# Optimization experiments

Hardware: AMD Instinct MI355X
Metric: run time of the kernel (lower is better)

Reference implementation:

```python
import jax, jax.numpy as jnp
import numpy as np

D = 256      # d_model
H = 8        # num heads
HD = D // H  # head dim
DFF = 1024   # feedforward dim
S = 1024     # seq len
B = 8        # batch
EPS = 1e-5


def _layernorm(x, g, b):
    mu = jnp.mean(x, axis=-1, keepdims=True)
    var = jnp.mean((x - mu) ** 2, axis=-1, keepdims=True)
    return (x - mu) * jax.lax.rsqrt(var + EPS) * g + b


def setup_inputs() -> dict:
    key = jax.random.key(0)
    ks = jax.random.split(key, 12)
    xav = lambda k, shape: jax.random.uniform(
        k, shape, jnp.float32, -1.0, 1.0) * np.sqrt(6.0 / (shape[0] + shape[-1]))
    return {
        "src": jax.random.normal(ks[0], (S, B, D), jnp.float32),
        "bias": jax.random.normal(ks[1], (B, H, S, S), jnp.float32),
        "in_proj_w": xav(ks[2], (3 * D, D)),
        "in_proj_b": jnp.zeros((3 * D,), jnp.float32),
        "out_w": xav(ks[3], (D, D)),
        "out_b": jnp.zeros((D,), jnp.float32),
        "w1": xav(ks[4], (DFF, D)),
        "b1": jnp.zeros((DFF,), jnp.float32),
        "w2": xav(ks[5], (D, DFF)),
        "b2": jnp.zeros((D,), jnp.float32),
        "g1": jnp.ones((D,), jnp.float32),
        "be1": jnp.zeros((D,), jnp.float32),
        "g2": jnp.ones((D,), jnp.float32),
        "be2": jnp.zeros((D,), jnp.float32),
    }


def reference(src, bias, in_proj_w, in_proj_b, out_w, out_b,
              w1, b1, w2, b2, g1, be1, g2, be2):
    # Pre-norm (note: residual uses the NORMED src, matching the torch code)
    x = _layernorm(src, g1, be1)                       # [S,B,D]
    qkv = x @ in_proj_w.T + in_proj_b                  # [S,B,3D]
    q, k, v = jnp.split(qkv, 3, axis=-1)
    q = q * (HD ** -0.5)
    # [S,B,D] -> [B,H,S,HD]
    to_heads = lambda t: t.reshape(S, B, H, HD).transpose(1, 2, 0, 3)
    qh, kh, vh = to_heads(q), to_heads(k), to_heads(v)
    scores = jnp.einsum('bhsd,bhtd->bhst', qh, kh) + bias
    attn = jax.nn.softmax(scores, axis=-1)             # [B,H,S,S]
    ctx = jnp.einsum('bhst,bhtd->bhsd', attn, vh)      # [B,H,S,HD]
    ctx = ctx.transpose(2, 0, 1, 3).reshape(S, B, D)
    attn_out = ctx @ out_w.T + out_b
    x = x + attn_out                                   # residual (eval: no dropout)
    y = _layernorm(x, g2, be2)
    ff = jax.nn.relu(y @ w1.T + b1) @ w2.T + b2
    return y + ff
```

## Files before the change

kernel.cpp:

```cpp
#include <hip/hip_runtime.h>
#include <hip/hip_bf16.h>
#include <cstdint>

typedef unsigned short u16;
typedef __attribute__((ext_vector_type(8))) short bf16x8;
typedef __attribute__((ext_vector_type(4))) float f32x4;

#define S_LEN 1024
#define BATCH 8
#define DMODEL 256
#define NHEAD 8
#define HDIM 32
#define DFF 1024
#define NROWS (S_LEN * BATCH)

static __device__ __forceinline__ u16 f2b(float f) {
    union { float f; unsigned u; } x{f};
    unsigned r = (x.u + 0x7fffu + ((x.u >> 16) & 1u)) >> 16;
    return (u16)r;
}

__global__ __launch_bounds__(256) void prep_kernel(
    const float* __restrict__ in, const float* __restrict__ g1,
    const float* __restrict__ be1, float* __restrict__ of, u16* __restrict__ ob,
    const float* __restrict__ ipw, const float* __restrict__ outw,
    const float* __restrict__ w1, const float* __restrict__ w2,
    const float* __restrict__ ipb,
    u16* __restrict__ wqkv, u16* __restrict__ wout,
    u16* __restrict__ w1b, u16* __restrict__ w2b, float* __restrict__ bq)
{
    const float s = 0.17677669529663689f;
    if (blockIdx.x >= 2048) {
        const int i4 = ((int)blockIdx.x - 2048) * 1024 + threadIdx.x * 4;
        const float* src; u16* dst; int off; float sc = 1.0f;
        if (i4 < 196608)      { src = ipw;  dst = wqkv; off = 0;      if (i4 < 65536) sc = s; }
        else if (i4 < 262144) { src = outw; dst = wout; off = 196608; }
        else if (i4 < 524288) { src = w1;   dst = w1b;  off = 262144; }
        else                  { src = w2;   dst = w2b;  off = 524288; }
        const float4 v = *(const float4*)(src + i4 - off);
        uint2 pk;
        pk.x = (unsigned)f2b(v.x * sc) | ((unsigned)f2b(v.y * sc) << 16);
        pk.y = (unsigned)f2b(v.z * sc) | ((unsigned)f2b(v.w * sc) << 16);
        *(uint2*)(dst + i4 - off) = pk;
        if (i4 < 768) {
            const float4 b = *(const float4*)(ipb + i4);
            const float bs = (i4 < 256) ? s : 1.0f;
            *(float4*)(bq + i4) = make_float4(b.x * bs, b.y * bs, b.z * bs, b.w * bs);
        }
        return;
    }
    const int w = threadIdx.x >> 6, l = threadIdx.x & 63;
    const int row = blockIdx.x * 4 + w;
    const float4 v = *(const float4*)(in + (size_t)row * DMODEL + l * 4);
    float s0 = v.x + v.y + v.z + v.w;
    #pragma unroll
    for (int o = 32; o; o >>= 1) s0 += __shfl_xor(s0, o);
    const float mu = s0 * (1.0f / DMODEL);
    const float dx = v.x - mu, dy = v.y - mu, dz = v.z - mu, dw = v.w - mu;
    float sq = dx * dx + dy * dy + dz * dz + dw * dw;
    #pragma unroll
    for (int o = 32; o; o >>= 1) sq += __shfl_xor(sq, o);
    const float rs = rsqrtf(sq * (1.0f / DMODEL) + 1e-5f);
    const float4 gv = *(const float4*)(g1 + l * 4);
    const float4 bv = *(const float4*)(be1 + l * 4);
    const float r0 = dx * rs * gv.x + bv.x;
    const float r1 = dy * rs * gv.y + bv.y;
    const float r2 = dz * rs * gv.z + bv.z;
    const float r3 = dw * rs * gv.w + bv.w;
    *(float4*)(of + (size_t)row * DMODEL + l * 4) = make_float4(r0, r1, r2, r3);
    uint2 pk;
    pk.x = (unsigned)f2b(r0) | ((unsigned)f2b(r1) << 16);
    pk.y = (unsigned)f2b(r2) | ((unsigned)f2b(r3) << 16);
    *(uint2*)(ob + (size_t)row * DMODEL + l * 4) = pk;
}

template <int MF>
__device__ __forceinline__ void gemm_core(
    const u16* __restrict__ A, const u16* __restrict__ Bw,
    int N, int K, int nbase, int rowbase, u16* sB, f32x4 acc[MF][4])
{
    const int tid = threadIdx.x, w = tid >> 6, l = tid & 63;
    const int g = l >> 4, q = l & 15;
    const u16* Arow = A + (size_t)(rowbase + w * (MF * 16) + q) * K + g * 8;

    const int sbr = tid >> 3, sseg = tid & 7;
    const size_t bsrc0 = (size_t)(nbase + sbr) * K + sseg * 8;
    const size_t bsrc1 = (size_t)(nbase + sbr + 32) * K + sseg * 8;
    const int d0 = sbr * 128 + ((sseg * 16) ^ ((sbr & 7) << 4));
    const int d1 = d0 + 32 * 128;

    {
        const uint4 r0 = *(const uint4*)(Bw + bsrc0);
        const uint4 r1 = *(const uint4*)(Bw + bsrc1);
        *(uint4*)((char*)sB + d0) = r0;
        *(uint4*)((char*)sB + d1) = r1;
    }
    const int NC = K >> 6;
    for (int c = 0; c < NC; ++c) {
        __syncthreads();
        char* sBc = (char*)sB + (c & 1) * 8192;
        char* sBn = (char*)sB + ((c + 1) & 1) * 8192;
        uint4 p0, p1;
        if (c + 1 < NC) {
            p0 = *(const uint4*)(Bw + bsrc0 + (c + 1) * 64);
            p1 = *(const uint4*)(Bw + bsrc1 + (c + 1) * 64);
        }
        const int kk = c * 64;
        #pragma unroll
        for (int ks = 0; ks < 2; ++ks) {
            bf16x8 af[MF];
            #pragma unroll
            for (int m = 0; m < MF; ++m)
                af[m] = *(const bf16x8*)(Arow + (size_t)m * 16 * K + kk + ks * 32);
            #pragma unroll
            for (int n = 0; n < 4; ++n) {
                const int rr = n * 16 + q;
                const bf16x8 bf = *(const bf16x8*)(
                    sBc + rr * 128 + ((ks * 64 + g * 16) ^ ((rr & 7) << 4)));
                #pragma unroll
                for (int m = 0; m < MF; ++m)
                    acc[m][n] = __builtin_amdgcn_mfma_f32_16x16x32_bf16(bf, af[m], acc[m][n], 0, 0, 0);
            }
        }
        if (c + 1 < NC) {
            *(uint4*)(sBn + d0) = p0;
            *(uint4*)(sBn + d1) = p1;
        }
    }
}

__global__ __launch_bounds__(256) void gemm_qkv(
    const u16* __restrict__ A, const u16* __restrict__ Bw,
    const float* __restrict__ bias,
    u16* __restrict__ Qh, u16* __restrict__ Kh, u16* __restrict__ Vt)
{
    __shared__ u16 sB[2][64 * 64];
    const int tid = threadIdx.x, w = tid >> 6, l = tid & 63;
    const int g = l >> 4, q = l & 15;
    const int rowbase = blockIdx.x * 128, nbase = blockIdx.y * 64;
    f32x4 acc[2][4] = {};
    gemm_core<2>(A, Bw, 768, 256, nbase, rowbase, &sB[0][0], acc);

    #pragma unroll
    for (int m = 0; m < 2; ++m) {
        const int row = rowbase + w * 32 + m * 16 + q;
        const int s = row >> 3, b = row & 7;
        if (nbase < 512) {
            u16* dst = (nbase >= 256) ? Kh : Qh;
            #pragma unroll
            for (int n = 0; n < 4; ++n) {
                const int col = nbase + n * 16 + g * 4;
                const float4 bv = *(const float4*)(bias + col);
                const int cc = col & 255, h = cc >> 5, hd = cc & 31;
                const int bh = b * 8 + h;
                uint2 pk;
                pk.x = (unsigned)f2b(acc[m][n][0] + bv.x) | ((unsigned)f2b(acc[m][n][1] + bv.y) << 16);
                pk.y = (unsigned)f2b(acc[m][n][2] + bv.z) | ((unsigned)f2b(acc[m][n][3] + bv.w) << 16);
                *(uint2*)(dst + ((size_t)bh * S_LEN + s) * HDIM + hd) = pk;
            }
        } else {
            #pragma unroll
            for (int n = 0; n < 4; ++n) {
                const int col = nbase + n * 16 + g * 4;
                const float4 bv = *(const float4*)(bias + col);
                const int cc = col - 512, h = cc >> 5, hd = cc & 31;
                const int bh = b * 8 + h;
                Vt[((size_t)bh * HDIM + hd + 0) * S_LEN + s] = f2b(acc[m][n][0] + bv.x);
                Vt[((size_t)bh * HDIM + hd + 1) * S_LEN + s] = f2b(acc[m][n][1] + bv.y);
                Vt[((size_t)bh * HDIM + hd + 2) * S_LEN + s] = f2b(acc[m][n][2] + bv.z);
                Vt[((size_t)bh * HDIM + hd + 3) * S_LEN + s] = f2b(acc[m][n][3] + bv.w);
            }
        }
    }
}

template <int MODE, int MF>
__global__ __launch_bounds__(256) void gemm_nt(
    const u16* __restrict__ A, const u16* __restrict__ Bw,
    const float* __restrict__ bias, const float* __restrict__ resid,
    float* __restrict__ outf, u16* __restrict__ outb,
    int N, int K)
{
    __shared__ u16 sB[2][64 * 64];
    const int tid = threadIdx.x, w = tid >> 6, l = tid & 63;
    const int g = l >> 4, q = l & 15;
    const int rowbase = blockIdx.x * (MF * 64), nbase = blockIdx.y * 64;
    f32x4 acc[MF][4] = {};
    gemm_core<MF>(A, Bw, N, K, nbase, rowbase, &sB[0][0], acc);

    #pragma unroll
    for (int m = 0; m < MF; ++m) {
        const int row = rowbase + w * (MF * 16) + m * 16 + q;
        #pragma unroll
        for (int n = 0; n < 4; ++n) {
            const int col = nbase + n * 16 + g * 4;
            const float4 bv = *(const float4*)(bias + col);
            float v0 = acc[m][n][0] + bv.x, v1 = acc[m][n][1] + bv.y;
            float v2 = acc[m][n][2] + bv.z, v3 = acc[m][n][3] + bv.w;
            if (MODE == 2) {
                v0 = fmaxf(v0, 0.f); v1 = fmaxf(v1, 0.f);
                v2 = fmaxf(v2, 0.f); v3 = fmaxf(v3, 0.f);
                uint2 pk;
                pk.x = (unsigned)f2b(v0) | ((unsigned)f2b(v1) << 16);
                pk.y = (unsigned)f2b(v2) | ((unsigned)f2b(v3) << 16);
                *(uint2*)(outb + (size_t)row * N + col) = pk;
            } else {
                const float4 rv = *(const float4*)(resid + (size_t)row * N + col);
                *(float4*)(outf + (size_t)row * N + col) =
                    make_float4(v0 + rv.x, v1 + rv.y, v2 + rv.z, v3 + rv.w);
            }
        }
    }
}

__global__ __launch_bounds__(256) void attn_kernel(
    const u16* __restrict__ Qh, const u16* __restrict__ Kh,
    const u16* __restrict__ Vt, const float* __restrict__ bias,
    u16* __restrict__ ctx)
{
    __shared__ u16 sK[2][64 * 32];
    __shared__ u16 sV[2][32 * 64];
    __shared__ u16 sP[4][16 * 64];
    const int tid = threadIdx.x, w = tid >> 6, l = tid & 63;
    const int g = l >> 4, q = l & 15;
    const int bh = blockIdx.y, b = bh >> 3, h = bh & 7;
    const int qbase = blockIdx.x * 64 + w * 16;
    const int qrow = qbase + q;

    const bf16x8 qf = *(const bf16x8*)(Qh + ((size_t)bh * S_LEN + qrow) * HDIM + g * 8);
    const float* brow = bias + ((size_t)bh * S_LEN + qrow) * S_LEN;
    u16* Pw = sP[w];
    const int swz = (q & 7) << 4;

    const u16* KsrcBase = Kh + ((size_t)bh * S_LEN + w * 16 + q) * HDIM + g * 8;
    const u16* VsrcBase = Vt + ((size_t)bh * HDIM + (w & 1) * 16 + q) * S_LEN
                             + (w >> 1) * 32 + g * 8;
    u16* KdstA = &sK[0][tid * 8]; u16* KdstB = &sK[1][tid * 8];
    u16* VdstA = &sV[0][tid * 8]; u16* VdstB = &sV[1][tid * 8];

    f32x4 ctxa[2] = {{0,0,0,0},{0,0,0,0}};
    float m = -1e30f, lsum = 0.f;

    auto loadB = [&](int kt, f32x4* bv) {
        #pragma unroll
        for (int n = 0; n < 4; ++n)
            bv[n] = __builtin_nontemporal_load(
                (const f32x4*)(brow + kt * 64 + n * 16 + g * 4));
    };

    auto proc = [&](int buf, const f32x4* bv) {
        f32x4 sc[4];
        #pragma unroll
        for (int n = 0; n < 4; ++n) {
            const bf16x8 kf = *(const bf16x8*)(&sK[buf][(n * 64 + l) * 8]);
            f32x4 z = {0, 0, 0, 0};
            sc[n] = __builtin_amdgcn_mfma_f32_16x16x32_bf16(kf, qf, z, 0, 0, 0);
        }
        #pragma unroll
        for (int n = 0; n < 4; ++n)
            #pragma unroll
            for (int r = 0; r < 4; ++r) sc[n][r] += bv[n][r];

        float mx = sc[0][0];
        #pragma unroll
        for (int n = 0; n < 4; ++n)
            #pragma unroll
            for (int r = 0; r < 4; ++r) mx = fmaxf(mx, sc[n][r]);
        mx = fmaxf(mx, __shfl_xor(mx, 16));
        mx = fmaxf(mx, __shfl_xor(mx, 32));
        const float mn = fmaxf(m, mx);
        const float corr = __expf(m - mn);
        float su = 0.f;
        u16 pb[16];
        #pragma unroll
        for (int n = 0; n < 4; ++n)
            #pragma unroll
            for (int r = 0; r < 4; ++r) {
                const float pv = __expf(sc[n][r] - mn);
                su += pv;
                pb[n * 4 + r] = f2b(pv);
            }
        su += __shfl_xor(su, 16);
        su += __shfl_xor(su, 32);
        lsum = lsum * corr + su;
        m = mn;
        #pragma unroll
        for (int jg = 0; jg < 2; ++jg)
            #pragma unroll
            for (int r = 0; r < 4; ++r) ctxa[jg][r] *= corr;

        #pragma unroll
        for (int n = 0; n < 4; ++n) {
            uint2 pk;
            pk.x = (unsigned)pb[n * 4] | ((unsigned)pb[n * 4 + 1] << 16);
            pk.y = (unsigned)pb[n * 4 + 2] | ((unsigned)pb[n * 4 + 3] << 16);
            *(uint2*)((char*)Pw + q * 128 + ((n * 32 + g * 8) ^ swz)) = pk;
        }

        #pragma unroll
        for (int ks = 0; ks < 2; ++ks) {
            const bf16x8 pf = *(const bf16x8*)((char*)Pw + q * 128 + ((ks * 64 + g * 16) ^ swz));
            #pragma unroll
            for (int jg = 0; jg < 2; ++jg) {
                const bf16x8 vf = *(const bf16x8*)(&sV[buf][((ks * 2 + jg) * 64 + l) * 8]);
                ctxa[jg] = __builtin_amdgcn_mfma_f32_16x16x32_bf16(vf, pf, ctxa[jg], 0, 0, 0);
            }
        }
    };

    f32x4 bv0[4], bv1[4];
    {
        const uint4 kr = *(const uint4*)(KsrcBase);
        const uint4 vr = *(const uint4*)(VsrcBase);
        *(uint4*)KdstA = kr;
        *(uint4*)VdstA = vr;
        loadB(0, bv0);
    }
    __syncthreads();

    for (int kt = 0; kt < 16; kt += 2) {
        {
            uint4 kr, vr;
            kr = *(const uint4*)(KsrcBase + (size_t)(kt + 1) * 64 * HDIM);
            vr = *(const uint4*)(VsrcBase + (size_t)(kt + 1) * 64);
            loadB(kt + 1, bv1);
            proc(0, bv0);
            *(uint4*)KdstB = kr;
            *(uint4*)VdstB = vr;
        }
        __syncthreads();
        {
            uint4 kr, vr;
            if (kt + 2 < 16) {
                kr = *(const uint4*)(KsrcBase + (size_t)(kt + 2) * 64 * HDIM);
                vr = *(const uint4*)(VsrcBase + (size_t)(kt + 2) * 64);
                loadB(kt + 2, bv0);
            }
            proc(1, bv1);
            if (kt + 2 < 16) {
                *(uint4*)KdstA = kr;
                *(uint4*)VdstA = vr;
            }
        }
        __syncthreads();
    }

    const float inv = 1.0f / lsum;
    #pragma unroll
    for (int jg = 0; jg < 2; ++jg) {
        uint2 pk;
        pk.x = (unsigned)f2b(ctxa[jg][0] * inv) | ((unsigned)f2b(ctxa[jg][1] * inv) << 16);
        pk.y = (unsigned)f2b(ctxa[jg][2] * inv) | ((unsigned)f2b(ctxa[jg][3] * inv) << 16);
        *(uint2*)(ctx + ((size_t)qrow * 8 + b) * DMODEL + h * 32 + jg * 16 + g * 4) = pk;
    }
}

__global__ __launch_bounds__(256) void oproj_ln(
    const u16* __restrict__ ctx, const u16* __restrict__ wob,
    const float* __restrict__ ob, const float* __restrict__ xf,
    const float* __restrict__ g2, const float* __restrict__ be2,
    float* __restrict__ yf, u16* __restrict__ yb)
{
    __shared__ float s1[4][16], s2[4][16];
    const int tid = threadIdx.x, wv = tid >> 6, l = tid & 63;
    const int g = l >> 4, q = l & 15;
    const int row = blockIdx.x * 16 + q;
    f32x4 acc[4] = {{0,0,0,0},{0,0,0,0},{0,0,0,0},{0,0,0,0}};
    const u16* Arow = ctx + (size_t)row * 256 + g * 8;
    const u16* Brow = wob + (size_t)(wv * 64 + q) * 256 + g * 8;

    #pragma unroll 2
    for (int kk = 0; kk < 256; kk += 32) {
        const bf16x8 af = *(const bf16x8*)(Arow + kk);
        #pragma unroll
        for (int n = 0; n < 4; ++n) {
            const bf16x8 bf = *(const bf16x8*)(Brow + (size_t)n * 16 * 256 + kk);
            acc[n] = __builtin_amdgcn_mfma_f32_16x16x32_bf16(bf, af, acc[n], 0, 0, 0);
        }
    }

    float sum = 0.f;
    #pragma unroll
    for (int n = 0; n < 4; ++n) {
        const int col = wv * 64 + n * 16 + g * 4;
        const float4 bv = *(const float4*)(ob + col);
        const float4 rv = *(const float4*)(xf + (size_t)row * 256 + col);
        acc[n][0] += bv.x + rv.x; acc[n][1] += bv.y + rv.y;
        acc[n][2] += bv.z + rv.z; acc[n][3] += bv.w + rv.w;
        sum += acc[n][0] + acc[n][1] + acc[n][2] + acc[n][3];
    }
    sum += __shfl_xor(sum, 16);
    sum += __shfl_xor(sum, 32);
    if (l < 16) s1[wv][q] = sum;
    __syncthreads();
    const float mu = (s1[0][q] + s1[1][q] + s1[2][q] + s1[3][q]) * (1.0f / 256);
    float sq = 0.f;
    #pragma unroll
    for (int n = 0; n < 4; ++n)
        #pragma unroll
        for (int r = 0; r < 4; ++r) {
            const float d = acc[n][r] - mu;
            sq += d * d;
        }
    sq += __shfl_xor(sq, 16);
    sq += __shfl_xor(sq, 32);
    if (l < 16) s2[wv][q] = sq;
    __syncthreads();
    const float rs = rsqrtf((s2[0][q] + s2[1][q] + s2[2][q] + s2[3][q]) * (1.0f / 256) + 1e-5f);

    #pragma unroll
    for (int n = 0; n < 4; ++n) {
        const int col = wv * 64 + n * 16 + g * 4;
        const float4 gv = *(const float4*)(g2 + col);
        const float4 b2 = *(const float4*)(be2 + col);
        const float y0 = (acc[n][0] - mu) * rs * gv.x + b2.x;
        const float y1 = (acc[n][1] - mu) * rs * gv.y + b2.y;
        const float y2 = (acc[n][2] - mu) * rs * gv.z + b2.z;
        const float y3 = (acc[n][3] - mu) * rs * gv.w + b2.w;
        *(float4*)(yf + (size_t)row * 256 + col) = make_float4(y0, y1, y2, y3);
        uint2 pk;
        pk.x = (unsigned)f2b(y0) | ((unsigned)f2b(y1) << 16);
        pk.y = (unsigned)f2b(y2) | ((unsigned)f2b(y3) << 16);
        *(uint2*)(yb + (size_t)row * 256 + col) = pk;
    }
}

extern "C" void kernel_launch(void* const* d_in, const int* in_sizes, int n_in,
                              void* d_out, int out_size, void* d_ws, size_t ws_size,
                              hipStream_t stream)
{
    const float* src  = (const float*)d_in[0];
    const float* bias = (const float*)d_in[1];
    const float* ipw  = (const float*)d_in[2];
    const float* ipb  = (const float*)d_in[3];
    const float* outw = (const float*)d_in[4];
    const float* outb = (const float*)d_in[5];
    const float* w1   = (const float*)d_in[6];
    const float* b1   = (const float*)d_in[7];
    const float* w2   = (const float*)d_in[8];
    const float* b2   = (const float*)d_in[9];
    const float* g1   = (const float*)d_in[10];
    const float* be1  = (const float*)d_in[11];
    const float* g2   = (const float*)d_in[12];
    const float* be2  = (const float*)d_in[13];

    char* p = (char*)d_ws;
    auto alloc = [&](size_t bytes) -> void* {
        void* r = (void*)p;
        p += (bytes + 255) & ~(size_t)255;
        return r;
    };
    float* xf   = (float*)alloc((size_t)NROWS * DMODEL * 4);
    u16*   xb   = (u16*)  alloc((size_t)NROWS * DMODEL * 2);
    u16*   Qh   = (u16*)  alloc((size_t)64 * S_LEN * HDIM * 2);
    u16*   Kb   = (u16*)  alloc((size_t)64 * S_LEN * HDIM * 2);
    u16*   Vt   = (u16*)  alloc((size_t)64 * S_LEN * HDIM * 2);
    u16*   ctx  = (u16*)  alloc((size_t)NROWS * DMODEL * 2);
    float* yf   = (float*)alloc((size_t)NROWS * DMODEL * 4);
    u16*   yb   = (u16*)  alloc((size_t)NROWS * DMODEL * 2);
    u16*   hb   = (u16*)  alloc((size_t)NROWS * DFF * 2);
    u16*   wqkv = (u16*)  alloc((size_t)768 * 256 * 2);
    u16*   wob  = (u16*)  alloc((size_t)256 * 256 * 2);
    u16*   w1b  = (u16*)  alloc((size_t)1024 * 256 * 2);
    u16*   w2b  = (u16*)  alloc((size_t)256 * 1024 * 2);
    float* bq   = (float*)alloc(768 * 4);

    prep_kernel<<<2816, 256, 0, stream>>>(src, g1, be1, xf, xb,
                                          ipw, outw, w1, w2, ipb,
                                          wqkv, wob, w1b, w2b, bq);
    gemm_qkv<<<dim3(64, 12), 256, 0, stream>>>(xb, wqkv, bq, Qh, Kb, Vt);
    attn_kernel<<<dim3(16, 64), 256, 0, stream>>>(Qh, Kb, Vt, bias, ctx);
    oproj_ln<<<512, 256, 0, stream>>>(ctx, wob, outb, xf, g2, be2, yf, yb);
    gemm_nt<2, 2><<<dim3(64, 16), 256, 0, stream>>>(yb, w1b, b1, nullptr, nullptr, hb, 1024, 256);
    gemm_nt<3, 1><<<dim3(128, 4), 256, 0, stream>>>(hb, w2b, b2, yf, (float*)d_out, nullptr, 256, 1024);
}
```

Before: 157.3 us.

## Fuse FFN up and down projections through shared memory; widen oproj tiles

Replaces the two separate FFN GEMM launches with one kernel. Each 512-thread block computes a 32-row slice of the ReLU hidden activations into a swizzled 64KB LDS buffer, then immediately runs the down-projection with the residual add. This removes the global round-trip of the 8192x1024 bf16 hidden tensor and one launch. The output-projection+LayerNorm kernel now handles 32 rows per block instead of 16. The trade-offs are only 256 blocks, large LDS per block limiting occupancy, and B operands read directly from global without LDS staging.

```diff
diff --git a/kernel.cpp b/kernel.cpp
--- a/kernel.cpp
+++ b/kernel.cpp
@@ -174,45 +174,6 @@
     }
 }
 
-template <int MODE, int MF>
-__global__ __launch_bounds__(256) void gemm_nt(
-    const u16* __restrict__ A, const u16* __restrict__ Bw,
-    const float* __restrict__ bias, const float* __restrict__ resid,
-    float* __restrict__ outf, u16* __restrict__ outb,
-    int N, int K)
-{
-    __shared__ u16 sB[2][64 * 64];
-    const int tid = threadIdx.x, w = tid >> 6, l = tid & 63;
-    const int g = l >> 4, q = l & 15;
-    const int rowbase = blockIdx.x * (MF * 64), nbase = blockIdx.y * 64;
-    f32x4 acc[MF][4] = {};
-    gemm_core<MF>(A, Bw, N, K, nbase, rowbase, &sB[0][0], acc);
-
-    #pragma unroll
-    for (int m = 0; m < MF; ++m) {
-        const int row = rowbase + w * (MF * 16) + m * 16 + q;
-        #pragma unroll
-        for (int n = 0; n < 4; ++n) {
-            const int col = nbase + n * 16 + g * 4;
-            const float4 bv = *(const float4*)(bias + col);
-            float v0 = acc[m][n][0] + bv.x, v1 = acc[m][n][1] + bv.y;
-            float v2 = acc[m][n][2] + bv.z, v3 = acc[m][n][3] + bv.w;
-            if (MODE == 2) {
-                v0 = fmaxf(v0, 0.f); v1 = fmaxf(v1, 0.f);
-                v2 = fmaxf(v2, 0.f); v3 = fmaxf(v3, 0.f);
-                uint2 pk;
-                pk.x = (unsigned)f2b(v0) | ((unsigned)f2b(v1) << 16);
-                pk.y = (unsigned)f2b(v2) | ((unsigned)f2b(v3) << 16);
-                *(uint2*)(outb + (size_t)row * N + col) = pk;
-            } else {
-                const float4 rv = *(const float4*)(resid + (size_t)row * N + col);
-                *(float4*)(outf + (size_t)row * N + col) =
-                    make_float4(v0 + rv.x, v1 + rv.y, v2 + rv.z, v3 + rv.w);
-            }
-        }
-    }
-}
-
 __global__ __launch_bounds__(256) void attn_kernel(
     const u16* __restrict__ Qh, const u16* __restrict__ Kh,
     const u16* __restrict__ Vt, const float* __restrict__ bias,
@@ -361,67 +322,181 @@
     const float* __restrict__ g2, const float* __restrict__ be2,
     float* __restrict__ yf, u16* __restrict__ yb)
 {
-    __shared__ float s1[4][16], s2[4][16];
+    __shared__ float s1[4][32], s2[4][32];
     const int tid = threadIdx.x, wv = tid >> 6, l = tid & 63;
     const int g = l >> 4, q = l & 15;
-    const int row = blockIdx.x * 16 + q;
-    f32x4 acc[4] = {{0,0,0,0},{0,0,0,0},{0,0,0,0},{0,0,0,0}};
-    const u16* Arow = ctx + (size_t)row * 256 + g * 8;
+    const int rowbase = blockIdx.x * 32;
+    f32x4 acc[2][4] = {};
+    const u16* Arow = ctx + (size_t)(rowbase + q) * 256 + g * 8;
     const u16* Brow = wob + (size_t)(wv * 64 + q) * 256 + g * 8;
 
     #pragma unroll 2
     for (int kk = 0; kk < 256; kk += 32) {
-        const bf16x8 af = *(const bf16x8*)(Arow + kk);
+        bf16x8 af[2];
+        #pragma unroll
+        for (int m = 0; m < 2; ++m)
+            af[m] = *(const bf16x8*)(Arow + (size_t)m * 16 * 256 + kk);
         #pragma unroll
         for (int n = 0; n < 4; ++n) {
             const bf16x8 bf = *(const bf16x8*)(Brow + (size_t)n * 16 * 256 + kk);
-            acc[n] = __builtin_amdgcn_mfma_f32_16x16x32_bf16(bf, af, acc[n], 0, 0, 0);
-        }
-    }
-
-    float sum = 0.f;
-    #pragma unroll
-    for (int n = 0; n < 4; ++n) {
-        const int col = wv * 64 + n * 16 + g * 4;
-        const float4 bv = *(const float4*)(ob + col);
-        const float4 rv = *(const float4*)(xf + (size_t)row * 256 + col);
-        acc[n][0] += bv.x + rv.x; acc[n][1] += bv.y + rv.y;
-        acc[n][2] += bv.z + rv.z; acc[n][3] += bv.w + rv.w;
-        sum += acc[n][0] + acc[n][1] + acc[n][2] + acc[n][3];
-    }
-    sum += __shfl_xor(sum, 16);
-    sum += __shfl_xor(sum, 32);
-    if (l < 16) s1[wv][q] = sum;
+            #pragma unroll
+            for (int m = 0; m < 2; ++m)
+                acc[m][n] = __builtin_amdgcn_mfma_f32_16x16x32_bf16(bf, af[m], acc[m][n], 0, 0, 0);
+        }
+    }
+
+    float sum[2] = {0.f, 0.f};
+    #pragma unroll
+    for (int m = 0; m < 2; ++m) {
+        const int row = rowbase + m * 16 + q;
+        #pragma unroll
+        for (int n = 0; n < 4; ++n) {
+            const int col = wv * 64 + n * 16 + g * 4;
+            const float4 bv = *(const float4*)(ob + col);
+            const float4 rv = *(const float4*)(xf + (size_t)row * 256 + col);
+            acc[m][n][0] += bv.x + rv.x; acc[m][n][1] += bv.y + rv.y;
+            acc[m][n][2] += bv.z + rv.z; acc[m][n][3] += bv.w + rv.w;
+            sum[m] += acc[m][n][0] + acc[m][n][1] + acc[m][n][2] + acc[m][n][3];
+        }
+        sum[m] += __shfl_xor(sum[m], 16);
+        sum[m] += __shfl_xor(sum[m], 32);
+    }
+    if (l < 16) { s1[wv][q] = sum[0]; s1[wv][16 + q] = sum[1]; }
     __syncthreads();
-    const float mu = (s1[0][q] + s1[1][q] + s1[2][q] + s1[3][q]) * (1.0f / 256);
-    float sq = 0.f;
-    #pragma unroll
-    for (int n = 0; n < 4; ++n)
-        #pragma unroll
-        for (int r = 0; r < 4; ++r) {
-            const float d = acc[n][r] - mu;
-            sq += d * d;
-        }
-    sq += __shfl_xor(sq, 16);
-    sq += __shfl_xor(sq, 32);
-    if (l < 16) s2[wv][q] = sq;
+    float mu[2], rs[2];
+    #pragma unroll
+    for (int m = 0; m < 2; ++m) {
+        const int lr = m * 16 + q;
+        mu[m] = (s1[0][lr] + s1[1][lr] + s1[2][lr] + s1[3][lr]) * (1.0f / 256);
+    }
+    float sq[2] = {0.f, 0.f};
+    #pragma unroll
+    for (int m = 0; m < 2; ++m) {
+        #pragma unroll
+        for (int n = 0; n < 4; ++n)
+            #pragma unroll
+            for (int r = 0; r < 4; ++r) {
+                const float d = acc[m][n][r] - mu[m];
+                sq[m] += d * d;
+            }
+        sq[m] += __shfl_xor(sq[m], 16);
+        sq[m] += __shfl_xor(sq[m], 32);
+    }
+    if (l < 16) { s2[wv][q] = sq[0]; s2[wv][16 + q] = sq[1]; }
     __syncthreads();
-    const float rs = rsqrtf((s2[0][q] + s2[1][q] + s2[2][q] + s2[3][q]) * (1.0f / 256) + 1e-5f);
-
-    #pragma unroll
-    for (int n = 0; n < 4; ++n) {
-        const int col = wv * 64 + n * 16 + g * 4;
-        const float4 gv = *(const float4*)(g2 + col);
-        const float4 b2 = *(const float4*)(be2 + col);
-        const float y0 = (acc[n][0] - mu) * rs * gv.x + b2.x;
-        const float y1 = (acc[n][1] - mu) * rs * gv.y + b2.y;
-        const float y2 = (acc[n][2] - mu) * rs * gv.z + b2.z;
-        const float y3 = (acc[n][3] - mu) * rs * gv.w + b2.w;
-        *(float4*)(yf + (size_t)row * 256 + col) = make_float4(y0, y1, y2, y3);
-        uint2 pk;
-        pk.x = (unsigned)f2b(y0) | ((unsigned)f2b(y1) << 16);
-        pk.y = (unsigned)f2b(y2) | ((unsigned)f2b(y3) << 16);
-        *(uint2*)(yb + (size_t)row * 256 + col) = pk;
+    #pragma unroll
+    for (int m = 0; m < 2; ++m) {
+        const int lr = m * 16 + q;
+        rs[m] = rsqrtf((s2[0][lr] + s2[1][lr] + s2[2][lr] + s2[3][lr]) * (1.0f / 256) + 1e-5f);
+    }
+
+    #pragma unroll
+    for (int m = 0; m < 2; ++m) {
+        const int row = rowbase + m * 16 + q;
+        #pragma unroll
+        for (int n = 0; n < 4; ++n) {
+            const int col = wv * 64 + n * 16 + g * 4;
+            const float4 gv = *(const float4*)(g2 + col);
+            const float4 b2 = *(const float4*)(be2 + col);
+            const float y0 = (acc[m][n][0] - mu[m]) * rs[m] * gv.x + b2.x;
+            const float y1 = (acc[m][n][1] - mu[m]) * rs[m] * gv.y + b2.y;
+            const float y2 = (acc[m][n][2] - mu[m]) * rs[m] * gv.z + b2.z;
+            const float y3 = (acc[m][n][3] - mu[m]) * rs[m] * gv.w + b2.w;
+            *(float4*)(yf + (size_t)row * 256 + col) = make_float4(y0, y1, y2, y3);
+            uint2 pk;
+            pk.x = (unsigned)f2b(y0) | ((unsigned)f2b(y1) << 16);
+            pk.y = (unsigned)f2b(y2) | ((unsigned)f2b(y3) << 16);
+            *(uint2*)(yb + (size_t)row * 256 + col) = pk;
+        }
+    }
+}
+
+__global__ __launch_bounds__(512) void ffn_fused(
+    const u16* __restrict__ yb, const u16* __restrict__ w1b,
+    const float* __restrict__ b1, const u16* __restrict__ w2b,
+    const float* __restrict__ b2, const float* __restrict__ yf,
+    float* __restrict__ out)
+{
+    __shared__ u16 sH[32 * 1024];
+    const int tid = threadIdx.x, w = tid >> 6, l = tid & 63;
+    const int g = l >> 4, q = l & 15;
+    const int rowbase = blockIdx.x * 32;
+
+    {
+        const int cbase = w * 128;
+        f32x4 acc[2][8] = {};
+        const u16* Arow = yb + (size_t)(rowbase + q) * 256 + g * 8;
+        const u16* Brow = w1b + (size_t)(cbase + q) * 256 + g * 8;
+        #pragma unroll 2
+        for (int kk = 0; kk < 256; kk += 32) {
+            bf16x8 af[2];
+            #pragma unroll
+            for (int m = 0; m < 2; ++m)
+                af[m] = *(const bf16x8*)(Arow + (size_t)m * 16 * 256 + kk);
+            #pragma unroll
+            for (int n = 0; n < 8; ++n) {
+                const bf16x8 bf = *(const bf16x8*)(Brow + (size_t)n * 16 * 256 + kk);
+                #pragma unroll
+                for (int m = 0; m < 2; ++m)
+                    acc[m][n] = __builtin_amdgcn_mfma_f32_16x16x32_bf16(bf, af[m], acc[m][n], 0, 0, 0);
+            }
+        }
+        #pragma unroll
+        for (int m = 0; m < 2; ++m) {
+            const int lr = m * 16 + q;
+            #pragma unroll
+            for (int n = 0; n < 8; ++n) {
+                const int col = cbase + n * 16 + g * 4;
+                const float4 bv = *(const float4*)(b1 + col);
+                const float v0 = fmaxf(acc[m][n][0] + bv.x, 0.f);
+                const float v1 = fmaxf(acc[m][n][1] + bv.y, 0.f);
+                const float v2 = fmaxf(acc[m][n][2] + bv.z, 0.f);
+                const float v3 = fmaxf(acc[m][n][3] + bv.w, 0.f);
+                uint2 pk;
+                pk.x = (unsigned)f2b(v0) | ((unsigned)f2b(v1) << 16);
+                pk.y = (unsigned)f2b(v2) | ((unsigned)f2b(v3) << 16);
+                const int x = col * 2;
+                const int sx = (x & ~127) | ((x & 127) ^ ((lr & 7) << 4));
+                *(uint2*)((char*)sH + lr * 2048 + sx) = pk;
+            }
+        }
+    }
+    __syncthreads();
+
+    {
+        const int obase = w * 32;
+        f32x4 acc[2][2] = {};
+        const u16* Brow = w2b + (size_t)(obase + q) * 1024 + g * 8;
+        for (int kk = 0; kk < 1024; kk += 32) {
+            bf16x8 af[2];
+            #pragma unroll
+            for (int m = 0; m < 2; ++m) {
+                const int lr = m * 16 + q;
+                const int x = (kk + g * 8) * 2;
+                const int sx = (x & ~127) | ((x & 127) ^ ((lr & 7) << 4));
+                af[m] = *(const bf16x8*)((char*)sH + lr * 2048 + sx);
+            }
+            #pragma unroll
+            for (int n = 0; n < 2; ++n) {
+                const bf16x8 bf = *(const bf16x8*)(Brow + (size_t)n * 16 * 1024 + kk);
+                #pragma unroll
+                for (int m = 0; m < 2; ++m)
+                    acc[m][n] = __builtin_amdgcn_mfma_f32_16x16x32_bf16(bf, af[m], acc[m][n], 0, 0, 0);
+            }
+        }
+        #pragma unroll
+        for (int m = 0; m < 2; ++m) {
+            const int row = rowbase + m * 16 + q;
+            #pragma unroll
+            for (int n = 0; n < 2; ++n) {
+                const int col = obase + n * 16 + g * 4;
+                const float4 bv = *(const float4*)(b2 + col);
+                const float4 rv = *(const float4*)(yf + (size_t)row * 256 + col);
+                *(float4*)(out + (size_t)row * 256 + col) = make_float4(
+                    acc[m][n][0] + bv.x + rv.x, acc[m][n][1] + bv.y + rv.y,
+                    acc[m][n][2] + bv.z + rv.z, acc[m][n][3] + bv.w + rv.w);
+            }
+        }
     }
 }
 
@@ -458,7 +533,6 @@
     u16*   ctx  = (u16*)  alloc((size_t)NROWS * DMODEL * 2);
     float* yf   = (float*)alloc((size_t)NROWS * DMODEL * 4);
     u16*   yb   = (u16*)  alloc((size_t)NROWS * DMODEL * 2);
-    u16*   hb   = (u16*)  alloc((size_t)NROWS * DFF * 2);
     u16*   wqkv = (u16*)  alloc((size_t)768 * 256 * 2);
     u16*   wob  = (u16*)  alloc((size_t)256 * 256 * 2);
     u16*   w1b  = (u16*)  alloc((size_t)1024 * 256 * 2);
@@ -470,7 +544,6 @@
                                           wqkv, wob, w1b, w2b, bq);
     gemm_qkv<<<dim3(64, 12), 256, 0, stream>>>(xb, wqkv, bq, Qh, Kb, Vt);
     attn_kernel<<<dim3(16, 64), 256, 0, stream>>>(Qh, Kb, Vt, bias, ctx);
-    oproj_ln<<<512, 256, 0, stream>>>(ctx, wob, outb, xf, g2, be2, yf, yb);
-    gemm_nt<2, 2><<<dim3(64, 16), 256, 0, stream>>>(yb, w1b, b1, nullptr, nullptr, hb, 1024, 256);
-    gemm_nt<3, 1><<<dim3(128, 4), 256, 0, stream>>>(hb, w2b, b2, yf, (float*)d_out, nullptr, 256, 1024);
-}
+    oproj_ln<<<256, 256, 0, stream>>>(ctx, wob, outb, xf, g2, be2, yf, yb);
+    ffn_fused<<<256, 512, 0, stream>>>(yb, w1b, b1, w2b, b2, yf, (float*)d_out);
+}
```

Result: no change. 158.9 us (+1.0%).
